# Kernel tuning notes

Hardware: AMD Instinct MI355X
Metric: run time of the kernel (lower is better)

## Reference

```python
import jax, jax.numpy as jnp
import numpy as np

N_NODES = 100000
N_EDGES = 1600000
C_IN = 32
C_OUT = 32


def setup_inputs() -> dict:
    key = jax.random.key(0)
    k1, k2, k3 = jax.random.split(key, 3)
    x = jax.random.normal(k1, (N_NODES, C_IN), dtype=jnp.float32)
    edge_index = jax.random.randint(k2, (2, N_EDGES), 0, N_NODES, dtype=jnp.int32)
    # Glorot-like init for the GCN linear weight [Cout, Cin]
    W = jax.random.normal(k3, (C_OUT, C_IN), dtype=jnp.float32) * (1.0 / np.sqrt(C_IN))
    b = jnp.zeros((C_OUT,), dtype=jnp.float32)
    return {"x": x, "edge_index": edge_index, "W": W, "b": b}


def reference(x, edge_index, W, b):
    # PyG GCNConv: add self-loops, symmetric normalization, linear, scatter-add, bias.
    n = x.shape[0]
    loops = jnp.arange(n, dtype=edge_index.dtype)
    row = jnp.concatenate([edge_index[0], loops])  # source nodes
    col = jnp.concatenate([edge_index[1], loops])  # target nodes

    # degree over targets (with self loops), deg^{-1/2} with inf -> 0
    ones = jnp.ones(row.shape[0], dtype=x.dtype)
    deg = jax.ops.segment_sum(ones, col, num_segments=n)
    dinv = jnp.where(deg > 0, jax.lax.rsqrt(jnp.maximum(deg, 1e-12)), 0.0)
    norm = dinv[row] * dinv[col]  # [E + N]

    h = x @ W.T  # [N, Cout] linear transform before propagation
    msg = h[row] * norm[:, None]  # gather + scale, [E+N, Cout]
    out = jax.ops.segment_sum(msg, col, num_segments=n)  # scatter-add to targets
    return out + b
```

## Files before the change

### kernel.cpp

```cpp
#include <hip/hip_runtime.h>

#define NN 100000
#define NE 1600000
#define C 32

#define SHIFT 8
#define BINW 256
#define NBIN ((NN + BINW - 1) / BINW)
#define EPB 8192
#define NCHK ((NE + EPB - 1) / EPB)
#define SLACK 56
#define CAPT (NCHK * SLACK)
#define SCAP 5120

__device__ __forceinline__ unsigned bf16rne(float f) {
    unsigned u = __float_as_uint(f);
    return (u + 0x7fffu + ((u >> 16) & 1u)) >> 16;
}
__device__ __forceinline__ float blo(unsigned u) { return __uint_as_float(u << 16); }
__device__ __forceinline__ float bhi(unsigned u) { return __uint_as_float(u & 0xffff0000u); }


__global__ __launch_bounds__(256) void k_bin(const int* __restrict__ ei,
                                             int* __restrict__ tmp,
                                             int* __restrict__ cfill) {
    __shared__ int lcur[NBIN];
    int b = blockIdx.x, t = threadIdx.x;
    for (int i = t; i < NBIN; i += 256) lcur[i] = i * CAPT + b * SLACK;
    __syncthreads();
    int e0 = b * EPB, e1 = min(e0 + EPB, NE);
    const int4* src4 = (const int4*)ei;
    const int4* col4 = (const int4*)(ei + NE);
    for (int q = (e0 >> 2) + t; q < (e1 >> 2); q += 256) {
        int4 s = src4[q];
        int4 c = col4[q];
        int p0 = atomicAdd(&lcur[c.x >> SHIFT], 1);
        tmp[p0] = (s.x << SHIFT) | (c.x & (BINW - 1));
        int p1 = atomicAdd(&lcur[c.y >> SHIFT], 1);
        tmp[p1] = (s.y << SHIFT) | (c.y & (BINW - 1));
        int p2 = atomicAdd(&lcur[c.z >> SHIFT], 1);
        tmp[p2] = (s.z << SHIFT) | (c.z & (BINW - 1));
        int p3 = atomicAdd(&lcur[c.w >> SHIFT], 1);
        tmp[p3] = (s.w << SHIFT) | (c.w & (BINW - 1));
    }
    __syncthreads();
    for (int i = t; i < NBIN; i += 256)
        cfill[b * NBIN + i] = lcur[i] - (i * CAPT + b * SLACK);
}

__global__ __launch_bounds__(1024) void k_deg(const int* __restrict__ cfill,
                                              const int* __restrict__ tmp,
                                              int* __restrict__ deg,
                                              float* __restrict__ dinv) {
    __shared__ int ccnt[NCHK];
    __shared__ int cnt[BINW];
    int bin = blockIdx.x, t = threadIdx.x;
    if (t < NCHK) ccnt[t] = cfill[t * NBIN + bin];
    if (t < BINW) cnt[t] = 0;
    __syncthreads();
    const int4* tp4 = (const int4*)tmp + bin * (CAPT >> 2);
    for (int q = t; q < (CAPT >> 2); q += 1024) {
        int4 v = tp4[q];
        int s = q << 2;
        int chunk = s / SLACK;
        int off = s - chunk * SLACK;
        if (off < ccnt[chunk]) atomicAdd(&cnt[v.x & (BINW - 1)], 1);
        if (++off == SLACK) { off = 0; ++chunk; }
        if (off < ccnt[chunk]) atomicAdd(&cnt[v.y & (BINW - 1)], 1);
        if (++off == SLACK) { off = 0; ++chunk; }
        if (off < ccnt[chunk]) atomicAdd(&cnt[v.z & (BINW - 1)], 1);
        if (++off == SLACK) { off = 0; ++chunk; }
        if (off < ccnt[chunk]) atomicAdd(&cnt[v.w & (BINW - 1)], 1);
    }
    __syncthreads();
    if (t < BINW) {
        int node = (bin << SHIFT) + t;
        if (node < NN) {
            int cv = cnt[t];
            deg[node] = cv;
            dinv[node] = rsqrtf(1.0f + (float)cv);
        }
    }
}

__global__ __launch_bounds__(256) void k_linear(const float* __restrict__ x,
                                                const float* __restrict__ W,
                                                const float* __restrict__ dinv,
                                                unsigned* __restrict__ hu) {
    __shared__ float Ws[C][C + 1];
    __shared__ float xs[16][C];
    int t = threadIdx.x;
    for (int i = t; i < C * C; i += 256)
        Ws[i / C][i % C] = W[i];

    int node0 = blockIdx.x * 16;
#pragma unroll
    for (int i = t; i < 16 * C; i += 256) {
        int idx = node0 * C + i;
        xs[i >> 5][i & 31] = (idx < NN * C) ? x[idx] : 0.0f;
    }
    __syncthreads();
    int lnode = t >> 4, m = t & 15;
    int node = node0 + lnode;
    if (node < NN) {
        float a0 = 0.0f, a1 = 0.0f;
#pragma unroll
        for (int k = 0; k < C; ++k) {
            float xv = xs[lnode][k];
            a0 += xv * Ws[2 * m][k];
            a1 += xv * Ws[2 * m + 1][k];
        }
        float d = dinv[node];
        hu[node * 16 + m] = bf16rne(a0 * d) | (bf16rne(a1 * d) << 16);
    }
}

#define AGG_T 1024
__global__ __launch_bounds__(AGG_T) void k_placeAgg(const int* __restrict__ cfill,
                                                    const int* __restrict__ tmp,
                                                    const int* __restrict__ deg,
                                                    const uint2* __restrict__ hu2,
                                                    const float* __restrict__ b,
                                                    float* __restrict__ out) {
    __shared__ int ccnt[NCHK];
    __shared__ int dg[BINW];
    __shared__ int lbase[BINW];
    __shared__ int lcur[BINW];
    __shared__ int lsort[SCAP];
    __shared__ int wtot[4], wbase[4];
    int bin = blockIdx.x, t = threadIdx.x;
    if (t < NCHK) ccnt[t] = cfill[t * NBIN + bin];
    if (t < BINW) {
        int node = (bin << SHIFT) + t;
        dg[t] = (node < NN) ? deg[node] : 0;
    }
    __syncthreads();
    int lane = t & 63, w4 = t >> 6;
    int cv = 0, v = 0;
    if (t < BINW) {
        cv = dg[t];
        v = cv;
#pragma unroll
        for (int d = 1; d < 64; d <<= 1) {
            int u = __shfl_up(v, d);
            if (lane >= d) v += u;
        }
        if (lane == 63) wtot[w4] = v;
    }
    __syncthreads();
    if (t == 0) {
        int r = 0;
#pragma unroll
        for (int k = 0; k < 4; ++k) { wbase[k] = r; r += wtot[k]; }
    }
    __syncthreads();
    if (t < BINW) {
        int loc = wbase[w4] + v - cv;
        lbase[t] = loc;
        lcur[t] = loc;
    }
    __syncthreads();
    const int4* tp4 = (const int4*)tmp + bin * (CAPT >> 2);
    for (int q = t; q < (CAPT >> 2); q += AGG_T) {
        int4 e = tp4[q];
        int s = q << 2;
        int chunk = s / SLACK;
        int off = s - chunk * SLACK;
        if (off < ccnt[chunk]) lsort[atomicAdd(&lcur[e.x & (BINW - 1)], 1)] = e.x >> SHIFT;
        if (++off == SLACK) { off = 0; ++chunk; }
        if (off < ccnt[chunk]) lsort[atomicAdd(&lcur[e.y & (BINW - 1)], 1)] = e.y >> SHIFT;
        if (++off == SLACK) { off = 0; ++chunk; }
        if (off < ccnt[chunk]) lsort[atomicAdd(&lcur[e.z & (BINW - 1)], 1)] = e.z >> SHIFT;
        if (++off == SLACK) { off = 0; ++chunk; }
        if (off < ccnt[chunk]) lsort[atomicAdd(&lcur[e.w & (BINW - 1)], 1)] = e.w >> SHIFT;
    }
    __syncthreads();
    int G = t >> 3, m = t & 7;
#pragma unroll
    for (int rr = 0; rr < 2; ++rr) {
        int loc = G + rr * 128;
        int node = (bin << SHIFT) + loc;
        int beg = lbase[loc], cnt = dg[loc];
        float s0 = 0.0f, s1 = 0.0f, s2 = 0.0f, s3 = 0.0f;
        int j = beg, jend = beg + cnt;
        for (; j + 3 < jend; j += 4) {
            int r0 = lsort[j], r1 = lsort[j + 1], r2 = lsort[j + 2], r3 = lsort[j + 3];
            uint2 u0 = hu2[r0 * 8 + m];
            uint2 u1 = hu2[r1 * 8 + m];
            uint2 u2 = hu2[r2 * 8 + m];
            uint2 u3 = hu2[r3 * 8 + m];
            s0 += blo(u0.x); s1 += bhi(u0.x); s2 += blo(u0.y); s3 += bhi(u0.y);
            s0 += blo(u1.x); s1 += bhi(u1.x); s2 += blo(u1.y); s3 += bhi(u1.y);
            s0 += blo(u2.x); s1 += bhi(u2.x); s2 += blo(u2.y); s3 += bhi(u2.y);
            s0 += blo(u3.x); s1 += bhi(u3.x); s2 += blo(u3.y); s3 += bhi(u3.y);
        }
        for (; j < jend; ++j) {
            uint2 u = hu2[lsort[j] * 8 + m];
            s0 += blo(u.x); s1 += bhi(u.x); s2 += blo(u.y); s3 += bhi(u.y);
        }
        if (node < NN) {
            float dn = rsqrtf(1.0f + (float)cnt);
            uint2 us = hu2[node * 8 + m];
            float4 bb = ((const float4*)b)[m];
            float o0 = bb.x + dn * (s0 + blo(us.x));
            float o1 = bb.y + dn * (s1 + bhi(us.x));
            float o2 = bb.z + dn * (s2 + blo(us.y));
            float o3 = bb.w + dn * (s3 + bhi(us.y));
            ((float4*)out)[node * 8 + m] = make_float4(o0, o1, o2, o3);
        }
    }
}


extern "C" void kernel_launch(void* const* d_in, const int* in_sizes, int n_in,
                              void* d_out, int out_size, void* d_ws, size_t ws_size,
                              hipStream_t stream) {
    const float* x  = (const float*)d_in[0];
    const int*   ei = (const int*)d_in[1];
    const float* W  = (const float*)d_in[2];
    const float* b  = (const float*)d_in[3];
    float* out = (float*)d_out;

    char* ws = (char*)d_ws;
    size_t o = 0;
    int*      tmp   = (int*)(ws + o);      o += (size_t)NBIN * CAPT * 4;   o = (o + 255) & ~(size_t)255;
    unsigned* hu    = (unsigned*)(ws + o); o += (size_t)NN * 16 * 4;       o = (o + 255) & ~(size_t)255;
    int*      cfill = (int*)(ws + o);      o += (size_t)NCHK * NBIN * 4;   o = (o + 255) & ~(size_t)255;
    int*      deg   = (int*)(ws + o);      o += (size_t)NN * 4;            o = (o + 255) & ~(size_t)255;
    float*    dinv  = (float*)(ws + o);

    k_bin<<<NCHK, 256, 0, stream>>>(ei, tmp, cfill);
    k_deg<<<NBIN, 1024, 0, stream>>>(cfill, tmp, deg, dinv);
    k_linear<<<(NN + 15) / 16, 256, 0, stream>>>(x, W, dinv, hu);
    k_placeAgg<<<NBIN, AGG_T, 0, stream>>>(cfill, tmp, deg, (const uint2*)hu, b, out);
}
```

Baseline: 125.8 us.

## Fuse degree counting with linear transform and widen binning blocks

Merges the degree-counting kernel and the linear-transform kernel into one per-bin kernel. Each block loads its bin's 256 node rows of x into shared memory, computes the degree counts, then produces the dinv-scaled bf16 h rows directly, so the dinv array and one kernel launch go away. The binning kernel also moves from 256 to 1024 threads per block. In exchange the fused kernel uses more shared memory (about 32KB for x plus W), which may lower occupancy, and it has only 391 blocks to do the matmul work.

```diff
diff --git a/kernel.cpp b/kernel.cpp
--- a/kernel.cpp
+++ b/kernel.cpp
@@ -21,17 +21,17 @@
 __device__ __forceinline__ float bhi(unsigned u) { return __uint_as_float(u & 0xffff0000u); }
 
 
-__global__ __launch_bounds__(256) void k_bin(const int* __restrict__ ei,
-                                             int* __restrict__ tmp,
-                                             int* __restrict__ cfill) {
+__global__ __launch_bounds__(1024) void k_bin(const int* __restrict__ ei,
+                                              int* __restrict__ tmp,
+                                              int* __restrict__ cfill) {
     __shared__ int lcur[NBIN];
     int b = blockIdx.x, t = threadIdx.x;
-    for (int i = t; i < NBIN; i += 256) lcur[i] = i * CAPT + b * SLACK;
+    if (t < NBIN) lcur[t] = t * CAPT + b * SLACK;
     __syncthreads();
     int e0 = b * EPB, e1 = min(e0 + EPB, NE);
     const int4* src4 = (const int4*)ei;
     const int4* col4 = (const int4*)(ei + NE);
-    for (int q = (e0 >> 2) + t; q < (e1 >> 2); q += 256) {
+    for (int q = (e0 >> 2) + t; q < (e1 >> 2); q += 1024) {
         int4 s = src4[q];
         int4 c = col4[q];
         int p0 = atomicAdd(&lcur[c.x >> SHIFT], 1);
@@ -44,19 +44,28 @@
         tmp[p3] = (s.w << SHIFT) | (c.w & (BINW - 1));
     }
     __syncthreads();
-    for (int i = t; i < NBIN; i += 256)
-        cfill[b * NBIN + i] = lcur[i] - (i * CAPT + b * SLACK);
-}
-
-__global__ __launch_bounds__(1024) void k_deg(const int* __restrict__ cfill,
-                                              const int* __restrict__ tmp,
-                                              int* __restrict__ deg,
-                                              float* __restrict__ dinv) {
+    if (t < NBIN)
+        cfill[b * NBIN + t] = lcur[t] - (t * CAPT + b * SLACK);
+}
+
+__global__ __launch_bounds__(1024) void k_degLin(const int* __restrict__ cfill,
+                                                 const int* __restrict__ tmp,
+                                                 const float* __restrict__ x,
+                                                 const float* __restrict__ W,
+                                                 int* __restrict__ deg,
+                                                 unsigned* __restrict__ hu) {
     __shared__ int ccnt[NCHK];
     __shared__ int cnt[BINW];
+    __shared__ float Ws[C][C + 1];
+    __shared__ float xs[BINW][C];
     int bin = blockIdx.x, t = threadIdx.x;
     if (t < NCHK) ccnt[t] = cfill[t * NBIN + bin];
     if (t < BINW) cnt[t] = 0;
+    Ws[t >> 5][t & 31] = W[t];
+    for (int i = t; i < BINW * C; i += 1024) {
+        int idx = (bin << SHIFT) * C + i;
+        xs[i >> 5][i & 31] = (idx < NN * C) ? x[idx] : 0.0f;
+    }
     __syncthreads();
     const int4* tp4 = (const int4*)tmp + bin * (CAPT >> 2);
     for (int q = t; q < (CAPT >> 2); q += 1024) {
@@ -75,43 +84,24 @@
     __syncthreads();
     if (t < BINW) {
         int node = (bin << SHIFT) + t;
+        if (node < NN) deg[node] = cnt[t];
+    }
+    int m = t & 15, nl0 = t >> 4;
+#pragma unroll
+    for (int rep = 0; rep < 4; ++rep) {
+        int nl = nl0 + (rep << 6);
+        int node = (bin << SHIFT) + nl;
         if (node < NN) {
-            int cv = cnt[t];
-            deg[node] = cv;
-            dinv[node] = rsqrtf(1.0f + (float)cv);
-        }
-    }
-}
-
-__global__ __launch_bounds__(256) void k_linear(const float* __restrict__ x,
-                                                const float* __restrict__ W,
-                                                const float* __restrict__ dinv,
-                                                unsigned* __restrict__ hu) {
-    __shared__ float Ws[C][C + 1];
-    __shared__ float xs[16][C];
-    int t = threadIdx.x;
-    for (int i = t; i < C * C; i += 256)
-        Ws[i / C][i % C] = W[i];
-
-    int node0 = blockIdx.x * 16;
-#pragma unroll
-    for (int i = t; i < 16 * C; i += 256) {
-        int idx = node0 * C + i;
-        xs[i >> 5][i & 31] = (idx < NN * C) ? x[idx] : 0.0f;
-    }
-    __syncthreads();
-    int lnode = t >> 4, m = t & 15;
-    int node = node0 + lnode;
-    if (node < NN) {
-        float a0 = 0.0f, a1 = 0.0f;
-#pragma unroll
-        for (int k = 0; k < C; ++k) {
-            float xv = xs[lnode][k];
-            a0 += xv * Ws[2 * m][k];
-            a1 += xv * Ws[2 * m + 1][k];
-        }
-        float d = dinv[node];
-        hu[node * 16 + m] = bf16rne(a0 * d) | (bf16rne(a1 * d) << 16);
+            float a0 = 0.0f, a1 = 0.0f;
+#pragma unroll
+            for (int k = 0; k < C; ++k) {
+                float xv = xs[nl][k];
+                a0 += xv * Ws[2 * m][k];
+                a1 += xv * Ws[2 * m + 1][k];
+            }
+            float d = rsqrtf(1.0f + (float)cnt[nl]);
+            hu[node * 16 + m] = bf16rne(a0 * d) | (bf16rne(a1 * d) << 16);
+        }
     }
 }
 
@@ -226,11 +216,9 @@
     int*      tmp   = (int*)(ws + o);      o += (size_t)NBIN * CAPT * 4;   o = (o + 255) & ~(size_t)255;
     unsigned* hu    = (unsigned*)(ws + o); o += (size_t)NN * 16 * 4;       o = (o + 255) & ~(size_t)255;
     int*      cfill = (int*)(ws + o);      o += (size_t)NCHK * NBIN * 4;   o = (o + 255) & ~(size_t)255;
-    int*      deg   = (int*)(ws + o);      o += (size_t)NN * 4;            o = (o + 255) & ~(size_t)255;
-    float*    dinv  = (float*)(ws + o);
-
-    k_bin<<<NCHK, 256, 0, stream>>>(ei, tmp, cfill);
-    k_deg<<<NBIN, 1024, 0, stream>>>(cfill, tmp, deg, dinv);
-    k_linear<<<(NN + 15) / 16, 256, 0, stream>>>(x, W, dinv, hu);
+    int*      deg   = (int*)(ws + o);
+
+    k_bin<<<NCHK, 1024, 0, stream>>>(ei, tmp, cfill);
+    k_degLin<<<NBIN, 1024, 0, stream>>>(cfill, tmp, x, W, deg, hu);
     k_placeAgg<<<NBIN, AGG_T, 0, stream>>>(cfill, tmp, deg, (const uint2*)hu, b, out);
 }
```

New measurement: 125.6 us. About the same (-0.2%).
